# Kernel tuning notes

Measured on AMD Instinct MI355X. Metric: run time of the kernel, lower is better.

## Reference

```python
import jax, jax.numpy as jnp
import numpy as np

B, L, E, H = 2, 2048, 1024, 16
HD = E // H


def _rel_shift(x):
    # x: [b, h, q, k] -> Transformer-XL relative shift via pad+reshape trick
    b, h, q, k = x.shape
    xp = jnp.pad(x, ((0, 0), (0, 0), (0, 0), (1, 0)))  # pad left of last dim
    xp = xp.reshape(b, h, k + 1, q)
    return xp[:, :, 1:, :].reshape(b, h, q, k)


def setup_inputs() -> dict:
    key = jax.random.key(0)
    ks = jax.random.split(key, 16)
    s = 0.02
    return {
        "query": jax.random.normal(ks[0], (B, L, E), jnp.float32),
        "key": jax.random.normal(ks[1], (B, L, E), jnp.float32),
        "value": jax.random.normal(ks[2], (B, L, E), jnp.float32),
        "pos_embedding": jax.random.normal(ks[3], (B, L, E), jnp.float32),
        "Wq": jax.random.normal(ks[4], (E, E), jnp.float32) * s,
        "bq": jnp.zeros((E,), jnp.float32),
        "Wk": jax.random.normal(ks[5], (E, E), jnp.float32) * s,
        "bk": jnp.zeros((E,), jnp.float32),
        "Wv": jax.random.normal(ks[6], (E, E), jnp.float32) * s,
        "bv": jnp.zeros((E,), jnp.float32),
        "Wp": jax.random.normal(ks[7], (E, E), jnp.float32) * s,  # Pos linear, no bias
        "Wo": jax.random.normal(ks[8], (E, E), jnp.float32) * s,
        "bo": jnp.zeros((E,), jnp.float32),
        "U": jax.random.normal(ks[9], (H, HD), jnp.float32) * s,
        "V": jax.random.normal(ks[10], (H, HD), jnp.float32) * s,
    }


def reference(query, key, value, pos_embedding, Wq, bq, Wk, bk, Wv, bv, Wp, Wo, bo, U, V):
    b, qlen, e = query.shape
    h, hd = U.shape
    scale = jnp.sqrt(jnp.asarray(e, query.dtype))
    # torch Linear: y = x @ W.T + b
    q = (query @ Wq.T + bq).reshape(b, qlen, h, hd)
    k = (key @ Wk.T + bk).reshape(b, key.shape[1], h, hd)
    v = (value @ Wv.T + bv).reshape(b, value.shape[1], h, hd)
    r = (pos_embedding @ Wp.T).reshape(b, -1, h, hd)
    content_score = jnp.einsum("bqhd,bkhd->bhqk", q + U, k)
    position_score = jnp.einsum("bqhd,bkhd->bhqk", q + V, r)
    position_score = _rel_shift(position_score)
    attention_score = (content_score + position_score) / scale
    # NOTE: the original module applies NO softmax; faithful reproduction.
    # einsum 'bhqk,bvhd->bqhd' sums over both k (scores) and v (values).
    alpha = jnp.einsum("bhqk,bvhd->bqhd", attention_score, v).reshape(b, qlen, e)
    return alpha @ Wo.T + bo
```

## Files before the change

### kernel.cpp

```cpp
#include <hip/hip_runtime.h>

#define BB 2
#define LL 2048
#define EE 1024
#define HH 16
#define HDD 64

typedef __bf16 bf16x8 __attribute__((ext_vector_type(8)));
typedef float f32x4 __attribute__((ext_vector_type(4)));

__device__ __forceinline__ unsigned short f2bf(float f) {
  unsigned int x = __float_as_uint(f);
  return (unsigned short)((x + 0x7FFFu + ((x >> 16) & 1u)) >> 16);
}

__device__ __forceinline__ float bf2f(unsigned short u) {
  return __uint_as_float((unsigned int)u << 16);
}

__device__ __forceinline__ void load_lds16(const void* g, void* l) {
  __builtin_amdgcn_global_load_lds(
      (const __attribute__((address_space(1))) void*)g,
      (__attribute__((address_space(3))) void*)l, 16, 0, 0);
}

#define SUMKV_BLOCKS 256
#define CAST_BLOCKS 1280
#define CAST_STRIDE (CAST_BLOCKS * 256)
__global__ __launch_bounds__(256) void prelude_kernel(
    const float* __restrict__ q, const float* __restrict__ pe,
    const float* __restrict__ wq, const float* __restrict__ wp,
    unsigned short* __restrict__ q16, unsigned short* __restrict__ pe16,
    unsigned short* __restrict__ wq16, unsigned short* __restrict__ wp16,
    const float* __restrict__ key, const float* __restrict__ value,
    float* __restrict__ keysum, float* __restrict__ valsum) {
  if (blockIdx.x < SUMKV_BLOCKS) {
    int blk2 = blockIdx.x;
    int b = blk2 >> 7, ch = blk2 & 127;
    int tid = threadIdx.x;
    const float4* k4 = (const float4*)(key   + ((size_t)b * LL + ch * 16) * EE);
    const float4* v4 = (const float4*)(value + ((size_t)b * LL + ch * 16) * EE);
    float4 ak = make_float4(0.f, 0.f, 0.f, 0.f);
    float4 av = make_float4(0.f, 0.f, 0.f, 0.f);
#pragma unroll 8
    for (int i = 0; i < 16; i++) {
      float4 kk = k4[i * 256 + tid];
      float4 vv = v4[i * 256 + tid];
      ak.x += kk.x; ak.y += kk.y; ak.z += kk.z; ak.w += kk.w;
      av.x += vv.x; av.y += vv.y; av.z += vv.z; av.w += vv.w;
    }
    int e = tid * 4;
    atomicAdd(&keysum[b * EE + e + 0], ak.x);
    atomicAdd(&keysum[b * EE + e + 1], ak.y);
    atomicAdd(&keysum[b * EE + e + 2], ak.z);
    atomicAdd(&keysum[b * EE + e + 3], ak.w);
    atomicAdd(&valsum[b * EE + e + 0], av.x);
    atomicAdd(&valsum[b * EE + e + 1], av.y);
    atomicAdd(&valsum[b * EE + e + 2], av.z);
    atomicAdd(&valsum[b * EE + e + 3], av.w);
  } else {
    const int NQ4 = BB * LL * EE / 4;
    const int NW4 = EE * EE / 4;
    int t = (blockIdx.x - SUMKV_BLOCKS) * 256 + threadIdx.x;
    float4 v[8]; unsigned short* dst[8]; int off[8];
#pragma unroll
    for (int k = 0; k < 8; k++) {
      int i = t + k * CAST_STRIDE;
      const float* src;
      if (i < NQ4)                { src = q;  dst[k] = q16;  off[k] = i; }
      else if (i < 2 * NQ4)       { src = pe; dst[k] = pe16; off[k] = i - NQ4; }
      else if (i < 2 * NQ4 + NW4) { src = wq; dst[k] = wq16; off[k] = i - 2 * NQ4; }
      else                        { src = wp; dst[k] = wp16; off[k] = i - 2 * NQ4 - NW4; }
      v[k] = ((const float4*)src)[off[k]];
    }
#pragma unroll
    for (int k = 0; k < 8; k++) {
      ushort4 u;
      u.x = f2bf(v[k].x); u.y = f2bf(v[k].y); u.z = f2bf(v[k].z); u.w = f2bf(v[k].w);
      ((ushort4*)dst[k])[off[k]] = u;
    }
  }
}

__global__ __launch_bounds__(256) void proj_kernel(
    const float* __restrict__ keysum, const float* __restrict__ valsum,
    const float* __restrict__ Wk, const float* __restrict__ bk,
    const float* __restrict__ Wv, const float* __restrict__ bv,
    float* __restrict__ Kproj, float* __restrict__ Vproj) {
  int wv = threadIdx.x >> 6, lane = threadIdx.x & 63;
  int idx = blockIdx.x * 4 + wv;
  int b = idx >> 10, ep = idx & (EE - 1);
  const float* sum  = blockIdx.z ? valsum : keysum;
  const float* W    = blockIdx.z ? Wv : Wk;
  const float* bias = blockIdx.z ? bv : bk;
  float* outp       = blockIdx.z ? Vproj : Kproj;
  float acc = 0.f;
  for (int k = lane; k < EE; k += 64) acc += sum[b * EE + k] * W[ep * EE + k];
  for (int off = 32; off; off >>= 1) acc += __shfl_down(acc, off, 64);
  if (lane == 0) outp[b * EE + ep] = acc + (float)LL * bias[ep];
}

__global__ __launch_bounds__(256, 5) void gemm_kernel(
    const unsigned short* __restrict__ q16, const unsigned short* __restrict__ wq16,
    const float* __restrict__ bq, unsigned short* __restrict__ qout,
    const unsigned short* __restrict__ pe16, const unsigned short* __restrict__ wp16,
    unsigned short* __restrict__ rout, float* __restrict__ chunks,
    const float* __restrict__ Vproj, const float* __restrict__ Wo,
    float* __restrict__ W2) {
  const int tid = threadIdx.x;
  const int lane = tid & 63;
  const int wv = tid >> 6;

  if (blockIdx.z == 2) {
    int bid = blockIdx.x + 32 * blockIdx.y;
    if (bid >= 256) return;
    int wslot = bid * 4 + wv;
    int base = wslot * 32;
    int b = base >> 14;
    int h = (base >> 10) & (HH - 1);
    int e0 = base & (EE - 1);
    float vp = Vproj[b * EE + h * HDD + lane];
    const float* wo = Wo + (size_t)e0 * EE + h * HDD + lane;
    for (int r = 0; r < 32; r++) {
      float acc = vp * wo[(size_t)r * EE];
      for (int off = 32; off; off >>= 1) acc += __shfl_down(acc, off, 64);
      if (lane == 0) W2[((size_t)b * HH + h) * EE + e0 + r] = acc;
    }
    return;
  }

  const int K = EE, N = EE;
  const unsigned short* X; const unsigned short* W; const float* bias;
  unsigned short* Out;
  if (blockIdx.z == 0) { X = q16;  W = wq16; bias = bq;      Out = qout; }
  else                 { X = pe16; W = wp16; bias = nullptr; Out = rout; }

  __shared__ __align__(16) unsigned short As[2][128 * 32];
  __shared__ __align__(16) unsigned short Bs[2][64 * 32];

  const int wm = wv >> 1, wn = wv & 1;
  const int m0 = blockIdx.x * 128;
  const int n0 = blockIdx.y * 64;

  const int srow_a = wv * 32 + (lane >> 2);
  const int srow_b = wv * 16 + (lane >> 2);
  const int s_src = ((lane & 3) - ((lane >> 3) & 3)) & 3;
  const unsigned short* gA = X + (size_t)(m0 + srow_a) * K + s_src * 8;
  const unsigned short* gB = W + (size_t)(n0 + srow_b) * K + s_src * 8;

  f32x4 acc[4][2];
#pragma unroll
  for (int i = 0; i < 4; i++)
#pragma unroll
    for (int j = 0; j < 2; j++) acc[i][j] = (f32x4)0.0f;

  const int arow = wm * 64 + (lane & 15);
  const int brow = wn * 32 + (lane & 15);
  const int koff = (((lane >> 4) + ((lane & 15) >> 1)) & 3) * 8;

#define GSTAGE(BI, KK)                                                    \
  do {                                                                    \
    load_lds16(gA + (KK),                  &As[BI][wv * 1024]);           \
    load_lds16(gA + (KK) + (size_t)16 * K, &As[BI][wv * 1024 + 512]);     \
    load_lds16(gB + (KK),                  &Bs[BI][wv * 512]);            \
  } while (0)

  GSTAGE(0, 0);
  __syncthreads();
  int bi = 0;
  for (int t = 0; t < K / 32; ++t) {
    if (t + 1 < K / 32) GSTAGE(bi ^ 1, (t + 1) * 32);
    bf16x8 af[4], bf[2];
#pragma unroll
    for (int i = 0; i < 4; i++)
      af[i] = *(const bf16x8*)&As[bi][(arow + i * 16) * 32 + koff];
#pragma unroll
    for (int j = 0; j < 2; j++)
      bf[j] = *(const bf16x8*)&Bs[bi][(brow + j * 16) * 32 + koff];
#pragma unroll
    for (int i = 0; i < 4; i++)
#pragma unroll
      for (int j = 0; j < 2; j++)
        acc[i][j] = __builtin_amdgcn_mfma_f32_16x16x32_bf16(af[i], bf[j], acc[i][j], 0, 0, 0);
    __syncthreads();
    bi ^= 1;
  }
#undef GSTAGE

  const int rbase = m0 + wm * 64 + (lane >> 4) * 4;
  const int cbase = n0 + wn * 32 + (lane & 15);
#pragma unroll
  for (int i = 0; i < 4; i++) {
#pragma unroll
    for (int j = 0; j < 2; j++) {
      int col = cbase + j * 16;
      float badd = bias ? bias[col] : 0.f;
#pragma unroll
      for (int g = 0; g < 4; g++) {
        int row = rbase + i * 16 + g;
        Out[(size_t)row * N + col] = f2bf(acc[i][j][g] + badd);
      }
    }
  }

  if (blockIdx.z == 1) {
    int b = m0 >> 11;
    int ch0 = ((m0 & (LL - 1)) >> 4) + wm * 4;
#pragma unroll
    for (int i = 0; i < 4; i++) {
#pragma unroll
      for (int j = 0; j < 2; j++) {
        float s = acc[i][j][0] + acc[i][j][1] + acc[i][j][2] + acc[i][j][3];
        s += __shfl_down(s, 32, 64);
        s += __shfl_down(s, 16, 64);
        if (lane < 16) {
          int col = n0 + wn * 32 + j * 16 + lane;
          chunks[((size_t)b * 128 + ch0 + i) * EE + col] = s;
        }
      }
    }
  }
}

__global__ __launch_bounds__(256) void scan2f_kernel(
    const unsigned short* __restrict__ qbuf, const unsigned short* __restrict__ rbuf,
    const float* __restrict__ chunks, const float* __restrict__ Kproj,
    const float* __restrict__ U, const float* __restrict__ V,
    float* __restrict__ S1, float* __restrict__ Dbuf) {
  int tid = threadIdx.x, lane = tid & 63;
  int hg = blockIdx.x, ch = blockIdx.y, b = blockIdx.z;
  int e = hg * 256 + tid;
  int h = hg * 4 + (tid >> 6);
  float pre = 0.f, tot = 0.f;
  for (int c = 0; c < 128; c++) {
    float cs = chunks[((size_t)b * 128 + c) * EE + e];
    tot += cs;
    if (c < ch) pre += cs;
  }
  float kp = Kproj[b * EE + e], Ue = U[e], Ve = V[e];
  float run = pre;
  size_t hoff = ((size_t)b * HH + h) * LL;
#pragma unroll 4
  for (int i = 0; i < 16; i++) {
    int m = ch * 16 + i;
    int p = LL - 1 - m;
    float qv = bf2f(qbuf[((size_t)b * LL + p) * EE + e]);
    float rv = bf2f(rbuf[((size_t)b * LL + m) * EE + e]);
    float tq = qv + Ve;
    float d = tq * run;
    float s = tq * tot + (qv + Ue) * kp;
#pragma unroll
    for (int off = 32; off; off >>= 1) {
      d += __shfl_down(d, off, 64);
      s += __shfl_down(s, off, 64);
    }
    if (lane == 0) { Dbuf[hoff + m] = d; S1[hoff + p] = s; }
    run += rv;
  }
}

__global__ __launch_bounds__(256) void out_kernel(
    const float* __restrict__ S1, const float* __restrict__ Dbuf,
    const float* __restrict__ W2, const float* __restrict__ bo,
    float* __restrict__ out) {
  int row0 = blockIdx.x * 8;
  int b = row0 >> 11, p0 = row0 & (LL - 1);
  int tid = threadIdx.x;
  __shared__ float sh[8][HH];
  if (tid < 128) {
    int rr = tid >> 4, h = tid & 15;
    int p = p0 + rr;
    size_t hoff = ((size_t)b * HH + h) * LL;
    float s1 = S1[hoff + p];
    float d1 = Dbuf[hoff + (LL - 1 - p)];
    float d2 = (p == LL - 1) ? 0.f : Dbuf[hoff + (LL - 2 - p)];
    sh[rr][h] = (s1 - d1 + d2) * (1.f / 32.f);
  }
  float4 w2r[HH];
#pragma unroll
  for (int h = 0; h < HH; h++)
    w2r[h] = ((const float4*)(W2 + ((size_t)b * HH + h) * EE))[tid];
  float4 bo4 = ((const float4*)bo)[tid];
  __syncthreads();
#pragma unroll
  for (int rr = 0; rr < 8; rr++) {
    float4 acc = bo4;
#pragma unroll
    for (int h = 0; h < HH; h++) {
      float s = sh[rr][h];
      acc.x += s * w2r[h].x; acc.y += s * w2r[h].y;
      acc.z += s * w2r[h].z; acc.w += s * w2r[h].w;
    }
    ((float4*)out)[(size_t)(row0 + rr) * 256 + tid] = acc;
  }
}

extern "C" void kernel_launch(void* const* d_in, const int* in_sizes, int n_in,
                              void* d_out, int out_size, void* d_ws, size_t ws_size,
                              hipStream_t stream) {
  const float* query = (const float*)d_in[0];
  const float* key   = (const float*)d_in[1];
  const float* value = (const float*)d_in[2];
  const float* pos   = (const float*)d_in[3];
  const float* Wq = (const float*)d_in[4];
  const float* bq = (const float*)d_in[5];
  const float* Wk = (const float*)d_in[6];
  const float* bk = (const float*)d_in[7];
  const float* Wv = (const float*)d_in[8];
  const float* bv = (const float*)d_in[9];
  const float* Wp = (const float*)d_in[10];
  const float* Wo = (const float*)d_in[11];
  const float* bo = (const float*)d_in[12];
  const float* U  = (const float*)d_in[13];
  const float* V  = (const float*)d_in[14];
  float* out = (float*)d_out;

  char* ws = (char*)d_ws;
  size_t o = 0;
  auto take = [&](size_t bytes) -> char* {
    char* p = ws + o;
    o += (bytes + 255) & ~(size_t)255;
    return p;
  };
  float* keysum = (float*)take(BB * EE * 4);
  float* valsum = (float*)take(BB * EE * 4);
  float* Kproj  = (float*)take(BB * EE * 4);
  float* Vproj  = (float*)take(BB * EE * 4);
  float* W2     = (float*)take((size_t)BB * HH * EE * 4);
  float* S1     = (float*)take((size_t)BB * HH * LL * 4);
  float* Dbuf   = (float*)take((size_t)BB * HH * LL * 4);
  float* chunks = (float*)take((size_t)BB * 128 * EE * 4);
  unsigned short* qbuf = (unsigned short*)take((size_t)BB * LL * EE * 2);
  unsigned short* rbuf = (unsigned short*)take((size_t)BB * LL * EE * 2);
  unsigned short* q16  = (unsigned short*)take((size_t)BB * LL * EE * 2);
  unsigned short* pe16 = (unsigned short*)take((size_t)BB * LL * EE * 2);
  unsigned short* wq16 = (unsigned short*)take((size_t)EE * EE * 2);
  unsigned short* wp16 = (unsigned short*)take((size_t)EE * EE * 2);

  hipMemsetAsync(keysum, 0, (size_t)2 * BB * EE * 4, stream);

  prelude_kernel<<<SUMKV_BLOCKS + CAST_BLOCKS, 256, 0, stream>>>(
      query, pos, Wq, Wp, q16, pe16, wq16, wp16, key, value, keysum, valsum);
  proj_kernel<<<dim3(BB * EE / 4, 1, 2), 256, 0, stream>>>(
      keysum, valsum, Wk, bk, Wv, bv, Kproj, Vproj);
  gemm_kernel<<<dim3(BB * LL / 128, EE / 64, 3), 256, 0, stream>>>(
      q16, wq16, bq, qbuf, pe16, wp16, rbuf, chunks, Vproj, Wo, W2);
  scan2f_kernel<<<dim3(4, 128, BB), 256, 0, stream>>>(qbuf, rbuf, chunks, Kproj, U, V, S1, Dbuf);
  out_kernel<<<dim3(BB * LL / 8), 256, 0, stream>>>(S1, Dbuf, W2, bo, out);
}
```

Baseline: 219.2 us.

## Load GEMM operands straight to registers and hoist chunk prefix sums into a kernel

The bf16 projection GEMM drops its LDS double-buffering. Each wave now computes a 64x64 tile from 16-byte global loads into registers, ping-ponged across two register sets, on 128x128 block tiles with a lower occupancy hint. A new small prefix kernel computes the per-chunk exclusive prefix and total of the chunk sums once, so the scan kernel no longer re-reads all 128 chunks in every block. The trade-off: operand sharing between waves now depends on the L1/L2 caches instead of LDS, there are fewer GEMM blocks, and the prefix kernel adds one very narrow serial launch.

```diff
diff --git a/kernel.cpp b/kernel.cpp
--- a/kernel.cpp
+++ b/kernel.cpp
@@ -16,12 +16,6 @@
 
 __device__ __forceinline__ float bf2f(unsigned short u) {
   return __uint_as_float((unsigned int)u << 16);
-}
-
-__device__ __forceinline__ void load_lds16(const void* g, void* l) {
-  __builtin_amdgcn_global_load_lds(
-      (const __attribute__((address_space(1))) void*)g,
-      (__attribute__((address_space(3))) void*)l, 16, 0, 0);
 }
 
 #define SUMKV_BLOCKS 256
@@ -100,7 +94,7 @@
   if (lane == 0) outp[b * EE + ep] = acc + (float)LL * bias[ep];
 }
 
-__global__ __launch_bounds__(256, 5) void gemm_kernel(
+__global__ __launch_bounds__(256, 3) void gemm_kernel(
     const unsigned short* __restrict__ q16, const unsigned short* __restrict__ wq16,
     const float* __restrict__ bq, unsigned short* __restrict__ qout,
     const unsigned short* __restrict__ pe16, const unsigned short* __restrict__ wp16,
@@ -113,7 +107,6 @@
 
   if (blockIdx.z == 2) {
     int bid = blockIdx.x + 32 * blockIdx.y;
-    if (bid >= 256) return;
     int wslot = bid * 4 + wv;
     int base = wslot * 32;
     int b = base >> 14;
@@ -135,64 +128,53 @@
   if (blockIdx.z == 0) { X = q16;  W = wq16; bias = bq;      Out = qout; }
   else                 { X = pe16; W = wp16; bias = nullptr; Out = rout; }
 
-  __shared__ __align__(16) unsigned short As[2][128 * 32];
-  __shared__ __align__(16) unsigned short Bs[2][64 * 32];
-
   const int wm = wv >> 1, wn = wv & 1;
-  const int m0 = blockIdx.x * 128;
-  const int n0 = blockIdx.y * 64;
-
-  const int srow_a = wv * 32 + (lane >> 2);
-  const int srow_b = wv * 16 + (lane >> 2);
-  const int s_src = ((lane & 3) - ((lane >> 3) & 3)) & 3;
-  const unsigned short* gA = X + (size_t)(m0 + srow_a) * K + s_src * 8;
-  const unsigned short* gB = W + (size_t)(n0 + srow_b) * K + s_src * 8;
-
-  f32x4 acc[4][2];
+  const int m0 = blockIdx.x * 128 + wm * 64;
+  const int n0 = blockIdx.y * 128 + wn * 64;
+
+  const unsigned short* pa = X + (size_t)(m0 + (lane & 15)) * K + (lane >> 4) * 8;
+  const unsigned short* pb = W + (size_t)(n0 + (lane & 15)) * K + (lane >> 4) * 8;
+
+  f32x4 acc[4][4];
 #pragma unroll
   for (int i = 0; i < 4; i++)
 #pragma unroll
-    for (int j = 0; j < 2; j++) acc[i][j] = (f32x4)0.0f;
-
-  const int arow = wm * 64 + (lane & 15);
-  const int brow = wn * 32 + (lane & 15);
-  const int koff = (((lane >> 4) + ((lane & 15) >> 1)) & 3) * 8;
-
-#define GSTAGE(BI, KK)                                                    \
+    for (int j = 0; j < 4; j++) acc[i][j] = (f32x4)0.0f;
+
+  bf16x8 aA[4], bA[4], aB[4], bB[4];
+
+#define LOADAB(AD, BD, T)                                                 \
   do {                                                                    \
-    load_lds16(gA + (KK),                  &As[BI][wv * 1024]);           \
-    load_lds16(gA + (KK) + (size_t)16 * K, &As[BI][wv * 1024 + 512]);     \
-    load_lds16(gB + (KK),                  &Bs[BI][wv * 512]);            \
+    _Pragma("unroll") for (int i = 0; i < 4; i++) {                       \
+      AD[i] = *(const bf16x8*)(pa + (size_t)i * 16 * K + (T) * 32);       \
+      BD[i] = *(const bf16x8*)(pb + (size_t)i * 16 * K + (T) * 32);       \
+    }                                                                     \
   } while (0)
-
-  GSTAGE(0, 0);
-  __syncthreads();
-  int bi = 0;
-  for (int t = 0; t < K / 32; ++t) {
-    if (t + 1 < K / 32) GSTAGE(bi ^ 1, (t + 1) * 32);
-    bf16x8 af[4], bf[2];
-#pragma unroll
-    for (int i = 0; i < 4; i++)
-      af[i] = *(const bf16x8*)&As[bi][(arow + i * 16) * 32 + koff];
-#pragma unroll
-    for (int j = 0; j < 2; j++)
-      bf[j] = *(const bf16x8*)&Bs[bi][(brow + j * 16) * 32 + koff];
-#pragma unroll
-    for (int i = 0; i < 4; i++)
-#pragma unroll
-      for (int j = 0; j < 2; j++)
-        acc[i][j] = __builtin_amdgcn_mfma_f32_16x16x32_bf16(af[i], bf[j], acc[i][j], 0, 0, 0);
-    __syncthreads();
-    bi ^= 1;
-  }
-#undef GSTAGE
-
-  const int rbase = m0 + wm * 64 + (lane >> 4) * 4;
-  const int cbase = n0 + wn * 32 + (lane & 15);
+#define MFMAS(AS, BS)                                                     \
+  do {                                                                    \
+    _Pragma("unroll") for (int i = 0; i < 4; i++)                         \
+    _Pragma("unroll") for (int j = 0; j < 4; j++)                         \
+      acc[i][j] = __builtin_amdgcn_mfma_f32_16x16x32_bf16(AS[i], BS[j],   \
+                                                          acc[i][j], 0, 0, 0); \
+  } while (0)
+
+  LOADAB(aA, bA, 0);
+#pragma unroll
+  for (int t = 0; t < 32; t += 2) {
+    if (t + 1 < 32) LOADAB(aB, bB, t + 1);
+    MFMAS(aA, bA);
+    if (t + 2 < 32) LOADAB(aA, bA, t + 2);
+    if (t + 1 < 32) MFMAS(aB, bB);
+  }
+#undef LOADAB
+#undef MFMAS
+
+  const int rbase = m0 + (lane >> 4) * 4;
+  const int cbase = n0 + (lane & 15);
 #pragma unroll
   for (int i = 0; i < 4; i++) {
 #pragma unroll
-    for (int j = 0; j < 2; j++) {
+    for (int j = 0; j < 4; j++) {
       int col = cbase + j * 16;
       float badd = bias ? bias[col] : 0.f;
 #pragma unroll
@@ -204,17 +186,18 @@
   }
 
   if (blockIdx.z == 1) {
-    int b = m0 >> 11;
-    int ch0 = ((m0 & (LL - 1)) >> 4) + wm * 4;
+    int b = (blockIdx.x * 128) >> 11;
+    int ch0 = (((blockIdx.x * 128) & (LL - 1)) >> 4) + wm * 4 + ((m0 & 64) ? 0 : 0);
+    ch0 = ((m0 & (LL - 1)) >> 4);
 #pragma unroll
     for (int i = 0; i < 4; i++) {
 #pragma unroll
-      for (int j = 0; j < 2; j++) {
+      for (int j = 0; j < 4; j++) {
         float s = acc[i][j][0] + acc[i][j][1] + acc[i][j][2] + acc[i][j][3];
         s += __shfl_down(s, 32, 64);
         s += __shfl_down(s, 16, 64);
         if (lane < 16) {
-          int col = n0 + wn * 32 + j * 16 + lane;
+          int col = n0 + j * 16 + lane;
           chunks[((size_t)b * 128 + ch0 + i) * EE + col] = s;
         }
       }
@@ -222,21 +205,31 @@
   }
 }
 
+__global__ __launch_bounds__(256) void prefix_kernel(
+    const float* __restrict__ chunks, float* __restrict__ pre,
+    float* __restrict__ tot) {
+  int b = blockIdx.x >> 2, hg = blockIdx.x & 3;
+  int e = hg * 256 + threadIdx.x;
+  float run = 0.f;
+  for (int c = 0; c < 128; c++) {
+    pre[((size_t)b * 128 + c) * EE + e] = run;
+    run += chunks[((size_t)b * 128 + c) * EE + e];
+  }
+  tot[b * EE + e] = run;
+}
+
 __global__ __launch_bounds__(256) void scan2f_kernel(
     const unsigned short* __restrict__ qbuf, const unsigned short* __restrict__ rbuf,
-    const float* __restrict__ chunks, const float* __restrict__ Kproj,
+    const float* __restrict__ preb, const float* __restrict__ totb,
+    const float* __restrict__ Kproj,
     const float* __restrict__ U, const float* __restrict__ V,
     float* __restrict__ S1, float* __restrict__ Dbuf) {
   int tid = threadIdx.x, lane = tid & 63;
   int hg = blockIdx.x, ch = blockIdx.y, b = blockIdx.z;
   int e = hg * 256 + tid;
   int h = hg * 4 + (tid >> 6);
-  float pre = 0.f, tot = 0.f;
-  for (int c = 0; c < 128; c++) {
-    float cs = chunks[((size_t)b * 128 + c) * EE + e];
-    tot += cs;
-    if (c < ch) pre += cs;
-  }
+  float pre = preb[((size_t)b * 128 + ch) * EE + e];
+  float tot = totb[b * EE + e];
   float kp = Kproj[b * EE + e], Ue = U[e], Ve = V[e];
   float run = pre;
   size_t hoff = ((size_t)b * HH + h) * LL;
@@ -330,6 +323,8 @@
   float* S1     = (float*)take((size_t)BB * HH * LL * 4);
   float* Dbuf   = (float*)take((size_t)BB * HH * LL * 4);
   float* chunks = (float*)take((size_t)BB * 128 * EE * 4);
+  float* pre    = (float*)take((size_t)BB * 128 * EE * 4);
+  float* tot    = (float*)take((size_t)BB * EE * 4);
   unsigned short* qbuf = (unsigned short*)take((size_t)BB * LL * EE * 2);
   unsigned short* rbuf = (unsigned short*)take((size_t)BB * LL * EE * 2);
   unsigned short* q16  = (unsigned short*)take((size_t)BB * LL * EE * 2);
@@ -343,8 +338,10 @@
       query, pos, Wq, Wp, q16, pe16, wq16, wp16, key, value, keysum, valsum);
   proj_kernel<<<dim3(BB * EE / 4, 1, 2), 256, 0, stream>>>(
       keysum, valsum, Wk, bk, Wv, bv, Kproj, Vproj);
-  gemm_kernel<<<dim3(BB * LL / 128, EE / 64, 3), 256, 0, stream>>>(
+  gemm_kernel<<<dim3(BB * LL / 128, EE / 128, 3), 256, 0, stream>>>(
       q16, wq16, bq, qbuf, pe16, wp16, rbuf, chunks, Vproj, Wo, W2);
-  scan2f_kernel<<<dim3(4, 128, BB), 256, 0, stream>>>(qbuf, rbuf, chunks, Kproj, U, V, S1, Dbuf);
+  prefix_kernel<<<dim3(4 * BB), 256, 0, stream>>>(chunks, pre, tot);
+  scan2f_kernel<<<dim3(4, 128, BB), 256, 0, stream>>>(
+      qbuf, rbuf, pre, tot, Kproj, U, V, S1, Dbuf);
   out_kernel<<<dim3(BB * LL / 8), 256, 0, stream>>>(S1, Dbuf, W2, bo, out);
 }
```

Result: slower. 259.9 us (+18.6%).
